# Kernel optimization log

Hardware: AMD Instinct MI355X
Metric: run time of the kernel (lower is better)

The kernel has to match this reference:

```python
import jax, jax.numpy as jnp
import numpy as np

WIDTH = 4096
NUM_HEADS = 8
BLOCK_W = WIDTH // NUM_HEADS


def _block_diag_linear(x, w, b):
    # x: [n, width] -> [n, h, bw]; w: [h, bw, bw]; b: [h, bw]
    n = x.shape[0]
    xh = x.reshape(n, NUM_HEADS, BLOCK_W)
    y = jnp.einsum('nhi,hij->nhj', xh, w) + b
    return y.reshape(n, WIDTH)


def setup_inputs() -> dict:
    key = jax.random.key(0)
    ks = jax.random.split(key, 7)
    n = 8192
    x = jax.random.normal(ks[0], (n, WIDTH), dtype=jnp.float32)
    s = jnp.sort(jax.random.randint(ks[1], (n,), 0, 8, dtype=jnp.int32))
    # a_param init: uniform on ring radii [0.9, 0.999], softplus-inverse transform
    eps = 1e-8
    u = jax.random.uniform(ks[2], (WIDTH,), minval=0.9**2 + eps, maxval=0.999**2 + eps)
    t = 0.5 * jnp.log(u)
    a_param = jnp.log(jnp.exp(-t) - 1.0).astype(jnp.float32)
    std = 1.0 / np.sqrt(BLOCK_W)
    ig_w = std * jax.random.normal(ks[3], (NUM_HEADS, BLOCK_W, BLOCK_W), dtype=jnp.float32)
    ig_b = jnp.zeros((NUM_HEADS, BLOCK_W), dtype=jnp.float32)
    ag_w = std * jax.random.normal(ks[4], (NUM_HEADS, BLOCK_W, BLOCK_W), dtype=jnp.float32)
    ag_b = jnp.zeros((NUM_HEADS, BLOCK_W), dtype=jnp.float32)
    return {'x': x, 's': s, 'a_param': a_param, 'ig_w': ig_w, 'ig_b': ig_b,
            'ag_w': ag_w, 'ag_b': ag_b}


def reference(x, s, a_param, ig_w, ig_b, ag_w, ag_b):
    n, k = x.shape
    # reset mask: True at position 0 and wherever segment id changes
    reset = jnp.concatenate([jnp.ones((1,), dtype=bool), s[1:] != s[:-1]])
    gate_x = jax.nn.sigmoid(_block_diag_linear(x, ig_w, ig_b))
    gate_a = jax.nn.sigmoid(_block_diag_linear(x, ag_w, ag_b))
    log_a = -8.0 * gate_a * jax.nn.softplus(a_param)  # [n, k]
    a = jnp.exp(log_a)
    a_square = jnp.exp(2.0 * log_a)
    multiplier = jnp.sqrt(1.0 - a_square)
    multiplier = jnp.where(reset[:, None], 1.0, multiplier)
    normalized_x = x * gate_x * multiplier
    # linear recurrence h[t] = a[t] * h[t-1] + normalized_x[t] via parallel scan
    def combine(e1, e2):
        a1, b1 = e1
        a2, b2 = e2
        return (a1 * a2, a2 * b1 + b2)
    _, out = jax.lax.associative_scan(combine, (a, normalized_x), axis=0)
    return out
```

## Files before the change

### kernel.cpp

```cpp
#include <hip/hip_runtime.h>
#include <hip/hip_bf16.h>
#include <stdint.h>

#define WIDTH 4096
#define NROWS 8192
#define NHEADS 8
#define BW 512
#define CS 128
#define NCHUNK (NROWS/CS)

typedef short bf16x8 __attribute__((ext_vector_type(8)));
typedef float f32x4 __attribute__((ext_vector_type(4)));

__device__ __forceinline__ uint32_t rne_bf16(float f) {
  uint32_t u = __float_as_uint(f);
  return (u + 0x7fffu + ((u >> 16) & 1u)) >> 16;
}
__device__ __forceinline__ uint32_t pack2(float lo, float hi) {
  return rne_bf16(lo) | (rne_bf16(hi) << 16);
}
__device__ __forceinline__ float bf16_to_f32(uint32_t bits) {
  return __uint_as_float(bits << 16);
}

__device__ __forceinline__ void gload_lds16(const void* g, void* l) {
  __builtin_amdgcn_global_load_lds(
      (const __attribute__((address_space(1))) void*)g,
      (__attribute__((address_space(3))) void*)l, 16, 0, 0);
}

__global__ void prep_xbf16(const float* __restrict__ x, uint16_t* __restrict__ xb) {
  size_t i = ((size_t)blockIdx.x * 256 + threadIdx.x) * 8;
  float4 f0 = *reinterpret_cast<const float4*>(x + i);
  float4 f1 = *reinterpret_cast<const float4*>(x + i + 4);
  uint4 v;
  v.x = pack2(f0.x, f0.y); v.y = pack2(f0.z, f0.w);
  v.z = pack2(f1.x, f1.y); v.w = pack2(f1.z, f1.w);
  *reinterpret_cast<uint4*>(xb + i) = v;
}

__global__ void prep_weights(const float* __restrict__ ig_w,
                             const float* __restrict__ ag_w,
                             uint16_t* __restrict__ wt) {
  __shared__ float tile[32][33];
  int j0 = blockIdx.x * 32;
  int i0 = blockIdx.y * 32;
  int m  = blockIdx.z;
  const float* src = ((m >> 3) ? ag_w : ig_w) + (size_t)(m & 7) * BW * BW;
  int tx = threadIdx.x & 31, ty = threadIdx.x >> 5;
  #pragma unroll
  for (int k = 0; k < 4; k++) {
    int i = i0 + ty + 8 * k;
    tile[ty + 8 * k][tx] = src[(size_t)i * BW + (j0 + tx)];
  }
  __syncthreads();
  #pragma unroll
  for (int k = 0; k < 4; k++) {
    int j = j0 + ty + 8 * k;
    wt[((size_t)m * BW + j) * BW + (i0 + tx)] = (uint16_t)rne_bf16(tile[tx][ty + 8 * k]);
  }
}

__global__ void prep_misc(const float* __restrict__ a_param, float* __restrict__ cvec) {
  int i = blockIdx.x * 256 + threadIdx.x;
  if (i < WIDTH) {
    float x = a_param[i];
    float sp = (x > 15.f) ? x : log1pf(expf(x));
    cvec[i] = 8.f * sp;
  }
}

#define BM 256
#define BN 128
#define BK 64

__global__ __launch_bounds__(512, 2)
void gates_gemm(const uint16_t* __restrict__ xb,
                const int* __restrict__ s,
                const uint16_t* __restrict__ wt,
                const float* __restrict__ ig_b,
                const float* __restrict__ ag_b,
                const float* __restrict__ cvec,
                uint32_t* __restrict__ lanx,
                float* __restrict__ cA,
                float* __restrict__ cB) {
  extern __shared__ __align__(16) unsigned char dsm[];
  __shared__ unsigned char resetm[BM];

  const int b = blockIdx.x;
  const int orig = (b & 7) * 128 + (b >> 3);
  const int h  = orig >> 7;
  const int rem = orig & 127;
  const int mt = rem >> 2;
  const int nt = rem & 3;
  const int m0 = mt * BM;
  const int j0 = nt * BN;

  const int tid = threadIdx.x;
  const int lane = tid & 63;
  const int w = tid >> 6;
  const int wr = w >> 1;
  const int wc = w & 1;
  const int lrow = lane & 15;
  const int lkg  = lane >> 4;

  if (tid < BM) {
    int n = m0 + tid;
    resetm[tid] = (n == 0) || (s[n] != s[n - 1]);
  }

  const char* xb_src[4];
  #pragma unroll
  for (int i = 0; i < 4; i++) {
    int o = (4 * w + i) * 1024 + (lane << 4);
    int row = o >> 7;
    int c = (o & 127) ^ ((row & 7) << 4);
    xb_src[i] = (const char*)xb + (size_t)(m0 + row) * (WIDTH * 2) + h * (BW * 2) + c;
  }
  const char* w_src[4];
  #pragma unroll
  for (int i = 0; i < 4; i++) {
    int o = (4 * w + i) * 1024 + (lane << 4);
    int g = o >> 14;
    int jl = (o >> 7) & 127;
    int c = (o & 127) ^ ((jl & 7) << 4);
    w_src[i] = (const char*)wt + ((size_t)((g * 8 + h) * BW + (j0 + jl))) * (BW * 2) + c;
  }

  f32x4 acc[2][4][4];
  #pragma unroll
  for (int g = 0; g < 2; g++)
    #pragma unroll
    for (int mf = 0; mf < 4; mf++)
      #pragma unroll
      for (int nf = 0; nf < 4; nf++)
        acc[g][mf][nf] = (f32x4){0.f, 0.f, 0.f, 0.f};

  {
    const int p0 = (2 * nt + 2) & 7;
    #pragma unroll
    for (int i = 0; i < 4; i++)
      gload_lds16(xb_src[i] + p0 * 128, dsm + (4 * w + i) * 1024);
    #pragma unroll
    for (int i = 0; i < 4; i++)
      gload_lds16(w_src[i] + p0 * 128, dsm + 32768 + (4 * w + i) * 1024);
  }
  __syncthreads();

  for (int kt = 0; kt < 8; kt++) {
    const uint32_t cbase = (uint32_t)(kt & 1) << 16;
    if (kt < 7) {
      const uint32_t nbase = cbase ^ 65536u;
      const int p = (2 * nt + 3 + kt) & 7;
      #pragma unroll
      for (int i = 0; i < 4; i++)
        gload_lds16(xb_src[i] + p * 128, dsm + nbase + (4 * w + i) * 1024);
      #pragma unroll
      for (int i = 0; i < 4; i++)
        gload_lds16(w_src[i] + p * 128, dsm + nbase + 32768 + (4 * w + i) * 1024);
    }
    #pragma unroll
    for (int ks = 0; ks < 2; ks++) {
      bf16x8 af[4];
      #pragma unroll
      for (int mf = 0; mf < 4; mf++) {
        int row = wr * 64 + 16 * mf + lrow;
        uint32_t addr = cbase + (uint32_t)((row << 7) + ks * 64 + lkg * 16);
        addr ^= (uint32_t)((row & 7) << 4);
        af[mf] = *reinterpret_cast<const bf16x8*>(dsm + addr);
      }
      #pragma unroll
      for (int g = 0; g < 2; g++) {
        #pragma unroll
        for (int nf = 0; nf < 4; nf++) {
          int j = wc * 64 + 16 * nf + lrow;
          uint32_t addr = cbase + (uint32_t)(32768 + (g << 14) + (j << 7) + ks * 64 + lkg * 16);
          addr ^= (uint32_t)((j & 7) << 4);
          bf16x8 bfr = *reinterpret_cast<const bf16x8*>(dsm + addr);
          #pragma unroll
          for (int mf = 0; mf < 4; mf++) {
            acc[g][mf][nf] = __builtin_amdgcn_mfma_f32_16x16x32_bf16(
                af[mf], bfr, acc[g][mf][nf], 0, 0, 0);
          }
        }
      }
    }
    __syncthreads();
  }

  float* smf = (float*)(dsm + 98304);

  #pragma unroll
  for (int nf = 0; nf < 4; nf++) {
    int jl = wc * 64 + 16 * nf + lrow;
    int jj = h * BW + j0 + jl;
    const uint32_t xsl = (uint32_t)(jl >> 6) << 16;
    const int cc2 = (jl & 63) * 2;
    float igb = ig_b[jj], agb = ag_b[jj], cv = cvec[jj];
    float segA[4], segB[4];
    #pragma unroll
    for (int mf = 0; mf < 4; mf++) {
      float A = 1.f, B = 0.f;
      int rbase = wr * 64 + 16 * mf + 4 * lkg;
      #pragma unroll
      for (int r = 0; r < 4; r++) {
        int row = rbase + r;
        int n = m0 + row;
        size_t o = (size_t)n * WIDTH + jj;
        float yig = acc[0][mf][nf][r] + igb;
        float yag = acc[1][mf][nf][r] + agb;
        float gx = __builtin_amdgcn_rcpf(1.f + __expf(-yig));
        float ga = __builtin_amdgcn_rcpf(1.f + __expf(-yag));
        float la = -ga * cv;
        uint32_t la_bits = rne_bf16(la);
        float la_r = bf16_to_f32(la_bits);
        float a = __expf(la_r);
        float mult = resetm[row] ? 1.f
                     : __builtin_amdgcn_sqrtf(fmaxf(1.f - a * a, 0.f));
        uint32_t xaddr = xsl + ((uint32_t)((row << 7) + cc2) ^ (uint32_t)((row & 7) << 4));
        float xv = bf16_to_f32(*reinterpret_cast<const uint16_t*>(dsm + xaddr));
        float nx = xv * gx * mult;
        uint32_t nx_bits = rne_bf16(nx);
        float nx_r = bf16_to_f32(nx_bits);
        lanx[o] = la_bits | (nx_bits << 16);
        A *= a;
        B = fmaf(a, B, nx_r);
      }
      segA[mf] = A; segB[mf] = B;
    }
    #pragma unroll
    for (int mf = 0; mf < 4; mf++) {
      float A = segA[mf], B = segB[mf];
      #pragma unroll
      for (int d = 16; d <= 32; d <<= 1) {
        float pA = __shfl_xor(A, d, 64);
        float pB = __shfl_xor(B, d, 64);
        bool up = (lane & d) != 0;
        B = up ? fmaf(A, pB, B) : fmaf(pA, B, pB);
        A *= pA;
      }
      segA[mf] = A; segB[mf] = B;
    }
    float colA = segA[0], colB = segB[0];
    #pragma unroll
    for (int mf = 1; mf < 4; mf++) {
      colB = fmaf(segA[mf], colB, segB[mf]);
      colA *= segA[mf];
    }
    if (lkg == 0) {
      int clocal = wc * 64 + 16 * nf + lrow;
      smf[wr * 128 + clocal] = colA;
      smf[512 + wr * 128 + clocal] = colB;
    }
  }
  __syncthreads();
  if (tid < 256) {
    int half = tid >> 7;
    int cl = tid & 127;
    int base = half * 2;
    float A0 = smf[base * 128 + cl],       B0 = smf[512 + base * 128 + cl];
    float A1 = smf[(base + 1) * 128 + cl], B1 = smf[512 + (base + 1) * 128 + cl];
    float Af = A0 * A1;
    float Bf = fmaf(A1, B0, B1);
    int ct = mt * 2 + half;
    int jj = h * BW + j0 + cl;
    cA[ct * WIDTH + jj] = Af;
    cB[ct * WIDTH + jj] = Bf;
  }
}

__global__ void scan_prefix(const float* __restrict__ cA, const float* __restrict__ cB,
                            float* __restrict__ prefix) {
  int c = blockIdx.x * 256 + threadIdx.x;
  float hcur = 0.f;
  for (int i0 = 0; i0 < NCHUNK; i0 += 8) {
    float av[8], bv[8];
    #pragma unroll
    for (int e = 0; e < 8; e++) { av[e] = cA[(i0 + e) * WIDTH + c]; bv[e] = cB[(i0 + e) * WIDTH + c]; }
    #pragma unroll
    for (int e = 0; e < 8; e++) { prefix[(i0 + e) * WIDTH + c] = hcur; hcur = av[e] * hcur + bv[e]; }
  }
}

__global__ void scan_apply(const uint32_t* __restrict__ lanx,
                           const float* __restrict__ prefix,
                           float* __restrict__ out) {
  int chunk = blockIdx.x;
  int c0 = (blockIdx.y * 256 + threadIdx.x) * 4;
  size_t base = (size_t)chunk * CS * WIDTH + c0;
  float h[4];
  #pragma unroll
  for (int q = 0; q < 4; q++) h[q] = prefix[chunk * WIDTH + c0 + q];
  for (int rb = 0; rb < CS; rb += 4) {
    uint4 v[4];
    #pragma unroll
    for (int e = 0; e < 4; e++)
      v[e] = *reinterpret_cast<const uint4*>(lanx + base + (size_t)(rb + e) * WIDTH);
    #pragma unroll
    for (int e = 0; e < 4; e++) {
      float4 ov;
      h[0] = fmaf(__expf(bf16_to_f32(v[e].x & 0xffffu)), h[0], bf16_to_f32(v[e].x >> 16)); ov.x = h[0];
      h[1] = fmaf(__expf(bf16_to_f32(v[e].y & 0xffffu)), h[1], bf16_to_f32(v[e].y >> 16)); ov.y = h[1];
      h[2] = fmaf(__expf(bf16_to_f32(v[e].z & 0xffffu)), h[2], bf16_to_f32(v[e].z >> 16)); ov.z = h[2];
      h[3] = fmaf(__expf(bf16_to_f32(v[e].w & 0xffffu)), h[3], bf16_to_f32(v[e].w >> 16)); ov.w = h[3];
      *reinterpret_cast<float4*>(out + base + (size_t)(rb + e) * WIDTH) = ov;
    }
  }
}

extern "C" void kernel_launch(void* const* d_in, const int* in_sizes, int n_in,
                              void* d_out, int out_size, void* d_ws, size_t ws_size,
                              hipStream_t stream) {
  const float* x       = (const float*)d_in[0];
  const int*   s       = (const int*)d_in[1];
  const float* a_param = (const float*)d_in[2];
  const float* ig_w    = (const float*)d_in[3];
  const float* ig_b    = (const float*)d_in[4];
  const float* ag_w    = (const float*)d_in[5];
  const float* ag_b    = (const float*)d_in[6];
  float* out = (float*)d_out;
  char* ws = (char*)d_ws;

  uint32_t* lanx   = (uint32_t*)ws;
  uint16_t* wt     = (uint16_t*)(ws + 134217728);
  uint16_t* xb     = (uint16_t*)(ws + 142606336);
  float*    cvec   = (float*)(ws + 209715200);
  float*    cA     = (float*)(ws + 209731584);
  float*    cB     = (float*)(ws + 210780160);
  float*    prefix = (float*)(ws + 211828736);

  prep_xbf16<<<dim3(16384), 256, 0, stream>>>(x, xb);
  prep_weights<<<dim3(16, 16, 16), 256, 0, stream>>>(ig_w, ag_w, wt);
  prep_misc<<<dim3(16), 256, 0, stream>>>(a_param, cvec);
  gates_gemm<<<dim3(1024), dim3(512), 131072, stream>>>(xb, s, wt, ig_b, ag_b, cvec,
                                                        lanx, cA, cB);
  scan_prefix<<<dim3(16), 256, 0, stream>>>(cA, cB, prefix);
  scan_apply<<<dim3(NCHUNK, 4), 256, 0, stream>>>(lanx, prefix, out);
}
```

Before: 236.1 us.

## Shrink gates GEMM tiles to 128x64 with single-buffered static LDS

Halves the GEMM tile in both dimensions (BM 256→128, BN 128→64), uses 256 threads per block with 4 blocks/CU, and launches 4096 blocks. The double-buffered 128KB dynamic LDS prefetch pipeline is replaced by a single 32KB static buffer, with a sync before and after each k-step load. The aim is higher occupancy and smaller per-block footprint so more waves hide memory latency. The cost is that global-to-LDS loads no longer overlap with MFMA work inside a block, and smaller tiles reload more of x and the weights from global memory.

```diff
diff --git a/kernel.cpp b/kernel.cpp
--- a/kernel.cpp
+++ b/kernel.cpp
@@ -70,11 +70,11 @@
   }
 }
 
-#define BM 256
-#define BN 128
+#define BM 128
+#define BN 64
 #define BK 64
 
-__global__ __launch_bounds__(512, 2)
+__global__ __launch_bounds__(256, 4)
 void gates_gemm(const uint16_t* __restrict__ xb,
                 const int* __restrict__ s,
                 const uint16_t* __restrict__ wt,
@@ -84,15 +84,15 @@
                 uint32_t* __restrict__ lanx,
                 float* __restrict__ cA,
                 float* __restrict__ cB) {
-  extern __shared__ __align__(16) unsigned char dsm[];
+  __shared__ __align__(16) unsigned char dsm[32768];
   __shared__ unsigned char resetm[BM];
 
   const int b = blockIdx.x;
-  const int orig = (b & 7) * 128 + (b >> 3);
-  const int h  = orig >> 7;
-  const int rem = orig & 127;
-  const int mt = rem >> 2;
-  const int nt = rem & 3;
+  const int orig = (b & 7) * 512 + (b >> 3);
+  const int h  = orig >> 9;
+  const int rem = orig & 511;
+  const int mt = rem >> 3;
+  const int nt = rem & 7;
   const int m0 = mt * BM;
   const int j0 = nt * BN;
 
@@ -112,7 +112,7 @@
   const char* xb_src[4];
   #pragma unroll
   for (int i = 0; i < 4; i++) {
-    int o = (4 * w + i) * 1024 + (lane << 4);
+    int o = i * 4096 + tid * 16;
     int row = o >> 7;
     int c = (o & 127) ^ ((row & 7) << 4);
     xb_src[i] = (const char*)xb + (size_t)(m0 + row) * (WIDTH * 2) + h * (BW * 2) + c;
@@ -120,61 +120,48 @@
   const char* w_src[4];
   #pragma unroll
   for (int i = 0; i < 4; i++) {
-    int o = (4 * w + i) * 1024 + (lane << 4);
-    int g = o >> 14;
-    int jl = (o >> 7) & 127;
+    int o = i * 4096 + tid * 16;
+    int g = o >> 13;
+    int jl = (o >> 7) & 63;
     int c = (o & 127) ^ ((jl & 7) << 4);
     w_src[i] = (const char*)wt + ((size_t)((g * 8 + h) * BW + (j0 + jl))) * (BW * 2) + c;
   }
 
-  f32x4 acc[2][4][4];
+  f32x4 acc[2][4][2];
   #pragma unroll
   for (int g = 0; g < 2; g++)
     #pragma unroll
     for (int mf = 0; mf < 4; mf++)
       #pragma unroll
-      for (int nf = 0; nf < 4; nf++)
+      for (int nf = 0; nf < 2; nf++)
         acc[g][mf][nf] = (f32x4){0.f, 0.f, 0.f, 0.f};
 
-  {
-    const int p0 = (2 * nt + 2) & 7;
+  for (int kt = 0; kt < 8; kt++) {
+    const int p = (nt + 1 + kt) & 7;
+    __syncthreads();
     #pragma unroll
     for (int i = 0; i < 4; i++)
-      gload_lds16(xb_src[i] + p0 * 128, dsm + (4 * w + i) * 1024);
+      gload_lds16(xb_src[i] + p * 128, dsm + i * 4096 + tid * 16);
     #pragma unroll
     for (int i = 0; i < 4; i++)
-      gload_lds16(w_src[i] + p0 * 128, dsm + 32768 + (4 * w + i) * 1024);
-  }
-  __syncthreads();
-
-  for (int kt = 0; kt < 8; kt++) {
-    const uint32_t cbase = (uint32_t)(kt & 1) << 16;
-    if (kt < 7) {
-      const uint32_t nbase = cbase ^ 65536u;
-      const int p = (2 * nt + 3 + kt) & 7;
-      #pragma unroll
-      for (int i = 0; i < 4; i++)
-        gload_lds16(xb_src[i] + p * 128, dsm + nbase + (4 * w + i) * 1024);
-      #pragma unroll
-      for (int i = 0; i < 4; i++)
-        gload_lds16(w_src[i] + p * 128, dsm + nbase + 32768 + (4 * w + i) * 1024);
-    }
+      gload_lds16(w_src[i] + p * 128, dsm + 16384 + i * 4096 + tid * 16);
+    __syncthreads();
     #pragma unroll
     for (int ks = 0; ks < 2; ks++) {
       bf16x8 af[4];
       #pragma unroll
       for (int mf = 0; mf < 4; mf++) {
         int row = wr * 64 + 16 * mf + lrow;
-        uint32_t addr = cbase + (uint32_t)((row << 7) + ks * 64 + lkg * 16);
+        uint32_t addr = (uint32_t)((row << 7) + ks * 64 + lkg * 16);
         addr ^= (uint32_t)((row & 7) << 4);
         af[mf] = *reinterpret_cast<const bf16x8*>(dsm + addr);
       }
       #pragma unroll
       for (int g = 0; g < 2; g++) {
         #pragma unroll
-        for (int nf = 0; nf < 4; nf++) {
-          int j = wc * 64 + 16 * nf + lrow;
-          uint32_t addr = cbase + (uint32_t)(32768 + (g << 14) + (j << 7) + ks * 64 + lkg * 16);
+        for (int nf = 0; nf < 2; nf++) {
+          int j = wc * 32 + 16 * nf + lrow;
+          uint32_t addr = (uint32_t)(16384 + (g << 13) + (j << 7) + ks * 64 + lkg * 16);
           addr ^= (uint32_t)((j & 7) << 4);
           bf16x8 bfr = *reinterpret_cast<const bf16x8*>(dsm + addr);
           #pragma unroll
@@ -185,17 +172,16 @@
         }
       }
     }
-    __syncthreads();
-  }
-
-  float* smf = (float*)(dsm + 98304);
-
-  #pragma unroll
-  for (int nf = 0; nf < 4; nf++) {
-    int jl = wc * 64 + 16 * nf + lrow;
+  }
+  __syncthreads();
+
+  float* smf = (float*)(dsm + 16384);
+
+  #pragma unroll
+  for (int nf = 0; nf < 2; nf++) {
+    int jl = wc * 32 + 16 * nf + lrow;
     int jj = h * BW + j0 + jl;
-    const uint32_t xsl = (uint32_t)(jl >> 6) << 16;
-    const int cc2 = (jl & 63) * 2;
+    const int cc2 = jl * 2;
     float igb = ig_b[jj], agb = ag_b[jj], cv = cvec[jj];
     float segA[4], segB[4];
     #pragma unroll
@@ -217,7 +203,7 @@
         float a = __expf(la_r);
         float mult = resetm[row] ? 1.f
                      : __builtin_amdgcn_sqrtf(fmaxf(1.f - a * a, 0.f));
-        uint32_t xaddr = xsl + ((uint32_t)((row << 7) + cc2) ^ (uint32_t)((row & 7) << 4));
+        uint32_t xaddr = (uint32_t)((row << 7) + cc2) ^ (uint32_t)((row & 7) << 4);
         float xv = bf16_to_f32(*reinterpret_cast<const uint16_t*>(dsm + xaddr));
         float nx = xv * gx * mult;
         uint32_t nx_bits = rne_bf16(nx);
@@ -248,24 +234,20 @@
       colA *= segA[mf];
     }
     if (lkg == 0) {
-      int clocal = wc * 64 + 16 * nf + lrow;
-      smf[wr * 128 + clocal] = colA;
-      smf[512 + wr * 128 + clocal] = colB;
+      int clocal = wc * 32 + 16 * nf + lrow;
+      smf[wr * 64 + clocal] = colA;
+      smf[128 + wr * 64 + clocal] = colB;
     }
   }
   __syncthreads();
-  if (tid < 256) {
-    int half = tid >> 7;
-    int cl = tid & 127;
-    int base = half * 2;
-    float A0 = smf[base * 128 + cl],       B0 = smf[512 + base * 128 + cl];
-    float A1 = smf[(base + 1) * 128 + cl], B1 = smf[512 + (base + 1) * 128 + cl];
+  if (tid < BN) {
+    float A0 = smf[tid],       B0 = smf[128 + tid];
+    float A1 = smf[64 + tid],  B1 = smf[192 + tid];
     float Af = A0 * A1;
     float Bf = fmaf(A1, B0, B1);
-    int ct = mt * 2 + half;
-    int jj = h * BW + j0 + cl;
-    cA[ct * WIDTH + jj] = Af;
-    cB[ct * WIDTH + jj] = Bf;
+    int jj = h * BW + j0 + tid;
+    cA[mt * WIDTH + jj] = Af;
+    cB[mt * WIDTH + jj] = Bf;
   }
 }
 
@@ -332,8 +314,8 @@
   prep_xbf16<<<dim3(16384), 256, 0, stream>>>(x, xb);
   prep_weights<<<dim3(16, 16, 16), 256, 0, stream>>>(ig_w, ag_w, wt);
   prep_misc<<<dim3(16), 256, 0, stream>>>(a_param, cvec);
-  gates_gemm<<<dim3(1024), dim3(512), 131072, stream>>>(xb, s, wt, ig_b, ag_b, cvec,
-                                                        lanx, cA, cB);
+  gates_gemm<<<dim3(4096), 256, 0, stream>>>(xb, s, wt, ig_b, ag_b, cvec,
+                                             lanx, cA, cB);
   scan_prefix<<<dim3(16), 256, 0, stream>>>(cA, cB, prefix);
   scan_apply<<<dim3(NCHUNK, 4), 256, 0, stream>>>(lanx, prefix, out);
 }
```

Measured after the change: 224.7 us. 1.05x faster.

## Shrink GEMM tile to 128 rows, single-buffer weights, fold log2e into exp2

Applied to the files above, without the earlier changes.

The gates GEMM tile drops from 256 to 128 rows with 256 threads and half the LDS, so more blocks can be resident. The weight tile is now single-buffered with separate load phases and two barriers per k-step, while x stays double-buffered with a two-ahead prefetch. LOG2E is folded into the weights, biases and the decay constant so every exp becomes exp2, and the epilogue loops are reordered so per-column constants are hoisted. The cost is that weight loads no longer overlap compute, there are extra barriers, and bf16 rounding now happens in log2 space.

```diff
diff --git a/kernel.cpp b/kernel.cpp
--- a/kernel.cpp
+++ b/kernel.cpp
@@ -8,6 +8,7 @@
 #define BW 512
 #define CS 128
 #define NCHUNK (NROWS/CS)
+#define LOG2E 1.4426950408889634f
 
 typedef short bf16x8 __attribute__((ext_vector_type(8)));
 typedef float f32x4 __attribute__((ext_vector_type(4)));
@@ -57,40 +58,41 @@
   #pragma unroll
   for (int k = 0; k < 4; k++) {
     int j = j0 + ty + 8 * k;
-    wt[((size_t)m * BW + j) * BW + (i0 + tx)] = (uint16_t)rne_bf16(tile[tx][ty + 8 * k]);
-  }
-}
-
-__global__ void prep_misc(const float* __restrict__ a_param, float* __restrict__ cvec) {
+    wt[((size_t)m * BW + j) * BW + (i0 + tx)] =
+        (uint16_t)rne_bf16(tile[tx][ty + 8 * k] * LOG2E);
+  }
+}
+
+__global__ void prep_misc(const float* __restrict__ a_param, float* __restrict__ cvec2) {
   int i = blockIdx.x * 256 + threadIdx.x;
   if (i < WIDTH) {
     float x = a_param[i];
     float sp = (x > 15.f) ? x : log1pf(expf(x));
-    cvec[i] = 8.f * sp;
-  }
-}
-
-#define BM 256
+    cvec2[i] = 8.f * sp * LOG2E;
+  }
+}
+
+#define BM 128
 #define BN 128
 #define BK 64
 
-__global__ __launch_bounds__(512, 2)
+__global__ __launch_bounds__(256, 2)
 void gates_gemm(const uint16_t* __restrict__ xb,
                 const int* __restrict__ s,
                 const uint16_t* __restrict__ wt,
                 const float* __restrict__ ig_b,
                 const float* __restrict__ ag_b,
-                const float* __restrict__ cvec,
+                const float* __restrict__ cvec2,
                 uint32_t* __restrict__ lanx,
                 float* __restrict__ cA,
                 float* __restrict__ cB) {
   extern __shared__ __align__(16) unsigned char dsm[];
-  __shared__ unsigned char resetm[BM];
+  unsigned char* resetm = dsm + 65536;
 
   const int b = blockIdx.x;
-  const int orig = (b & 7) * 128 + (b >> 3);
-  const int h  = orig >> 7;
-  const int rem = orig & 127;
+  const int orig = (b & 7) * 256 + (b >> 3);
+  const int h  = orig >> 8;
+  const int rem = orig & 255;
   const int mt = rem >> 2;
   const int nt = rem & 3;
   const int m0 = mt * BM;
@@ -112,15 +114,15 @@
   const char* xb_src[4];
   #pragma unroll
   for (int i = 0; i < 4; i++) {
-    int o = (4 * w + i) * 1024 + (lane << 4);
+    int o = i * 4096 + tid * 16;
     int row = o >> 7;
     int c = (o & 127) ^ ((row & 7) << 4);
     xb_src[i] = (const char*)xb + (size_t)(m0 + row) * (WIDTH * 2) + h * (BW * 2) + c;
   }
-  const char* w_src[4];
-  #pragma unroll
-  for (int i = 0; i < 4; i++) {
-    int o = (4 * w + i) * 1024 + (lane << 4);
+  const char* w_src[8];
+  #pragma unroll
+  for (int i = 0; i < 8; i++) {
+    int o = i * 4096 + tid * 16;
     int g = o >> 14;
     int jl = (o >> 7) & 127;
     int c = (o & 127) ^ ((jl & 7) << 4);
@@ -138,27 +140,21 @@
 
   {
     const int p0 = (2 * nt + 2) & 7;
+    const int p1 = (2 * nt + 3) & 7;
     #pragma unroll
     for (int i = 0; i < 4; i++)
-      gload_lds16(xb_src[i] + p0 * 128, dsm + (4 * w + i) * 1024);
+      gload_lds16(xb_src[i] + p0 * 128, dsm + i * 4096 + tid * 16);
     #pragma unroll
     for (int i = 0; i < 4; i++)
-      gload_lds16(w_src[i] + p0 * 128, dsm + 32768 + (4 * w + i) * 1024);
+      gload_lds16(xb_src[i] + p1 * 128, dsm + 16384 + i * 4096 + tid * 16);
+    #pragma unroll
+    for (int i = 0; i < 8; i++)
+      gload_lds16(w_src[i] + p0 * 128, dsm + 32768 + i * 4096 + tid * 16);
   }
   __syncthreads();
 
   for (int kt = 0; kt < 8; kt++) {
-    const uint32_t cbase = (uint32_t)(kt & 1) << 16;
-    if (kt < 7) {
-      const uint32_t nbase = cbase ^ 65536u;
-      const int p = (2 * nt + 3 + kt) & 7;
-      #pragma unroll
-      for (int i = 0; i < 4; i++)
-        gload_lds16(xb_src[i] + p * 128, dsm + nbase + (4 * w + i) * 1024);
-      #pragma unroll
-      for (int i = 0; i < 4; i++)
-        gload_lds16(w_src[i] + p * 128, dsm + nbase + 32768 + (4 * w + i) * 1024);
-    }
+    const uint32_t cbase = (uint32_t)(kt & 1) << 14;
     #pragma unroll
     for (int ks = 0; ks < 2; ks++) {
       bf16x8 af[4];
@@ -174,7 +170,7 @@
         #pragma unroll
         for (int nf = 0; nf < 4; nf++) {
           int j = wc * 64 + 16 * nf + lrow;
-          uint32_t addr = cbase + (uint32_t)(32768 + (g << 14) + (j << 7) + ks * 64 + lkg * 16);
+          uint32_t addr = (uint32_t)(32768 + (g << 14) + (j << 7) + ks * 64 + lkg * 16);
           addr ^= (uint32_t)((j & 7) << 4);
           bf16x8 bfr = *reinterpret_cast<const bf16x8*>(dsm + addr);
           #pragma unroll
@@ -186,51 +182,77 @@
       }
     }
     __syncthreads();
-  }
-
-  float* smf = (float*)(dsm + 98304);
-
+    if (kt < 7) {
+      const int pw = (2 * nt + 3 + kt) & 7;
+      #pragma unroll
+      for (int i = 0; i < 8; i++)
+        gload_lds16(w_src[i] + pw * 128, dsm + 32768 + i * 4096 + tid * 16);
+    }
+    if (kt < 6) {
+      const int px = (2 * nt + 4 + kt) & 7;
+      const uint32_t nb = cbase;
+      #pragma unroll
+      for (int i = 0; i < 4; i++)
+        gload_lds16(xb_src[i] + px * 128, dsm + nb + i * 4096 + tid * 16);
+    }
+    __syncthreads();
+  }
+
+  float* smf = (float*)(dsm + 32768);
+
+  float igb[4], agb[4], cv2[4];
   #pragma unroll
   for (int nf = 0; nf < 4; nf++) {
-    int jl = wc * 64 + 16 * nf + lrow;
-    int jj = h * BW + j0 + jl;
-    const uint32_t xsl = (uint32_t)(jl >> 6) << 16;
-    const int cc2 = (jl & 63) * 2;
-    float igb = ig_b[jj], agb = ag_b[jj], cv = cvec[jj];
-    float segA[4], segB[4];
-    #pragma unroll
-    for (int mf = 0; mf < 4; mf++) {
-      float A = 1.f, B = 0.f;
-      int rbase = wr * 64 + 16 * mf + 4 * lkg;
-      #pragma unroll
-      for (int r = 0; r < 4; r++) {
-        int row = rbase + r;
-        int n = m0 + row;
-        size_t o = (size_t)n * WIDTH + jj;
-        float yig = acc[0][mf][nf][r] + igb;
-        float yag = acc[1][mf][nf][r] + agb;
-        float gx = __builtin_amdgcn_rcpf(1.f + __expf(-yig));
-        float ga = __builtin_amdgcn_rcpf(1.f + __expf(-yag));
-        float la = -ga * cv;
-        uint32_t la_bits = rne_bf16(la);
+    int jj = h * BW + j0 + wc * 64 + 16 * nf + lrow;
+    igb[nf] = ig_b[jj] * LOG2E;
+    agb[nf] = ag_b[jj] * LOG2E;
+    cv2[nf] = cvec2[jj];
+  }
+
+  const uint32_t xhalf = (uint32_t)wc << 14;
+  float segA[4][4], segB[4][4];
+  #pragma unroll
+  for (int mf = 0; mf < 4; mf++) {
+    float A[4] = {1.f, 1.f, 1.f, 1.f}, B[4] = {0.f, 0.f, 0.f, 0.f};
+    int rbase = wr * 64 + 16 * mf + 4 * lkg;
+    #pragma unroll
+    for (int r = 0; r < 4; r++) {
+      int row = rbase + r;
+      int n = m0 + row;
+      bool rs = resetm[row] != 0;
+      uint32_t xswz = (uint32_t)((row & 7) << 4);
+      #pragma unroll
+      for (int nf = 0; nf < 4; nf++) {
+        int cloc = 16 * nf + lrow;
+        size_t o = (size_t)n * WIDTH + h * BW + j0 + wc * 64 + cloc;
+        float yig = acc[0][mf][nf][r] + igb[nf];
+        float yag = acc[1][mf][nf][r] + agb[nf];
+        float gx = __builtin_amdgcn_rcpf(1.f + exp2f(-yig));
+        float ga = __builtin_amdgcn_rcpf(1.f + exp2f(-yag));
+        float la2 = -ga * cv2[nf];
+        uint32_t la_bits = rne_bf16(la2);
         float la_r = bf16_to_f32(la_bits);
-        float a = __expf(la_r);
-        float mult = resetm[row] ? 1.f
+        float a = exp2f(la_r);
+        float mult = rs ? 1.f
                      : __builtin_amdgcn_sqrtf(fmaxf(1.f - a * a, 0.f));
-        uint32_t xaddr = xsl + ((uint32_t)((row << 7) + cc2) ^ (uint32_t)((row & 7) << 4));
+        uint32_t xaddr = xhalf + (uint32_t)(row << 7) + (((uint32_t)(cloc * 2)) ^ xswz);
         float xv = bf16_to_f32(*reinterpret_cast<const uint16_t*>(dsm + xaddr));
         float nx = xv * gx * mult;
         uint32_t nx_bits = rne_bf16(nx);
         float nx_r = bf16_to_f32(nx_bits);
         lanx[o] = la_bits | (nx_bits << 16);
-        A *= a;
-        B = fmaf(a, B, nx_r);
+        A[nf] *= a;
+        B[nf] = fmaf(a, B[nf], nx_r);
       }
-      segA[mf] = A; segB[mf] = B;
-    }
+    }
+    #pragma unroll
+    for (int nf = 0; nf < 4; nf++) { segA[nf][mf] = A[nf]; segB[nf][mf] = B[nf]; }
+  }
+  #pragma unroll
+  for (int nf = 0; nf < 4; nf++) {
     #pragma unroll
     for (int mf = 0; mf < 4; mf++) {
-      float A = segA[mf], B = segB[mf];
+      float A = segA[nf][mf], B = segB[nf][mf];
       #pragma unroll
       for (int d = 16; d <= 32; d <<= 1) {
         float pA = __shfl_xor(A, d, 64);
@@ -239,33 +261,29 @@
         B = up ? fmaf(A, pB, B) : fmaf(pA, B, pB);
         A *= pA;
       }
-      segA[mf] = A; segB[mf] = B;
-    }
-    float colA = segA[0], colB = segB[0];
+      segA[nf][mf] = A; segB[nf][mf] = B;
+    }
+    float colA = segA[nf][0], colB = segB[nf][0];
     #pragma unroll
     for (int mf = 1; mf < 4; mf++) {
-      colB = fmaf(segA[mf], colB, segB[mf]);
-      colA *= segA[mf];
+      colB = fmaf(segA[nf][mf], colB, segB[nf][mf]);
+      colA *= segA[nf][mf];
     }
     if (lkg == 0) {
       int clocal = wc * 64 + 16 * nf + lrow;
       smf[wr * 128 + clocal] = colA;
-      smf[512 + wr * 128 + clocal] = colB;
+      smf[256 + wr * 128 + clocal] = colB;
     }
   }
   __syncthreads();
-  if (tid < 256) {
-    int half = tid >> 7;
-    int cl = tid & 127;
-    int base = half * 2;
-    float A0 = smf[base * 128 + cl],       B0 = smf[512 + base * 128 + cl];
-    float A1 = smf[(base + 1) * 128 + cl], B1 = smf[512 + (base + 1) * 128 + cl];
+  if (tid < BN) {
+    float A0 = smf[tid],        B0 = smf[256 + tid];
+    float A1 = smf[128 + tid],  B1 = smf[384 + tid];
     float Af = A0 * A1;
     float Bf = fmaf(A1, B0, B1);
-    int ct = mt * 2 + half;
-    int jj = h * BW + j0 + cl;
-    cA[ct * WIDTH + jj] = Af;
-    cB[ct * WIDTH + jj] = Bf;
+    int jj = h * BW + j0 + tid;
+    cA[mt * WIDTH + jj] = Af;
+    cB[mt * WIDTH + jj] = Bf;
   }
 }
 
@@ -299,10 +317,10 @@
     #pragma unroll
     for (int e = 0; e < 4; e++) {
       float4 ov;
-      h[0] = fmaf(__expf(bf16_to_f32(v[e].x & 0xffffu)), h[0], bf16_to_f32(v[e].x >> 16)); ov.x = h[0];
-      h[1] = fmaf(__expf(bf16_to_f32(v[e].y & 0xffffu)), h[1], bf16_to_f32(v[e].y >> 16)); ov.y = h[1];
-      h[2] = fmaf(__expf(bf16_to_f32(v[e].z & 0xffffu)), h[2], bf16_to_f32(v[e].z >> 16)); ov.z = h[2];
-      h[3] = fmaf(__expf(bf16_to_f32(v[e].w & 0xffffu)), h[3], bf16_to_f32(v[e].w >> 16)); ov.w = h[3];
+      h[0] = fmaf(exp2f(bf16_to_f32(v[e].x & 0xffffu)), h[0], bf16_to_f32(v[e].x >> 16)); ov.x = h[0];
+      h[1] = fmaf(exp2f(bf16_to_f32(v[e].y & 0xffffu)), h[1], bf16_to_f32(v[e].y >> 16)); ov.y = h[1];
+      h[2] = fmaf(exp2f(bf16_to_f32(v[e].z & 0xffffu)), h[2], bf16_to_f32(v[e].z >> 16)); ov.z = h[2];
+      h[3] = fmaf(exp2f(bf16_to_f32(v[e].w & 0xffffu)), h[3], bf16_to_f32(v[e].w >> 16)); ov.w = h[3];
       *reinterpret_cast<float4*>(out + base + (size_t)(rb + e) * WIDTH) = ov;
     }
   }
@@ -324,16 +342,16 @@
   uint32_t* lanx   = (uint32_t*)ws;
   uint16_t* wt     = (uint16_t*)(ws + 134217728);
   uint16_t* xb     = (uint16_t*)(ws + 142606336);
-  float*    cvec   = (float*)(ws + 209715200);
+  float*    cvec2  = (float*)(ws + 209715200);
   float*    cA     = (float*)(ws + 209731584);
   float*    cB     = (float*)(ws + 210780160);
   float*    prefix = (float*)(ws + 211828736);
 
   prep_xbf16<<<dim3(16384), 256, 0, stream>>>(x, xb);
   prep_weights<<<dim3(16, 16, 16), 256, 0, stream>>>(ig_w, ag_w, wt);
-  prep_misc<<<dim3(16), 256, 0, stream>>>(a_param, cvec);
-  gates_gemm<<<dim3(1024), dim3(512), 131072, stream>>>(xb, s, wt, ig_b, ag_b, cvec,
-                                                        lanx, cA, cB);
+  prep_misc<<<dim3(16), 256, 0, stream>>>(a_param, cvec2);
+  gates_gemm<<<dim3(2048), dim3(256), 65664, stream>>>(xb, s, wt, ig_b, ag_b, cvec2,
+                                                       lanx, cA, cB);
   scan_prefix<<<dim3(16), 256, 0, stream>>>(cA, cB, prefix);
   scan_apply<<<dim3(NCHUNK, 4), 256, 0, stream>>>(lanx, prefix, out);
 }
```

After: 228.0 us. 3.4% less time.
